# Optimization experiments

Hardware: AMD Instinct MI355X
Metric: run time of the kernel (lower is better)

## Reference

```python
import jax, jax.numpy as jnp
import numpy as np

B, T, D, UNITS = 32, 2048, 1024, 1024


def setup_inputs() -> dict:
    key = jax.random.key(0)
    ks = jax.random.split(key, 9)
    values = jax.random.normal(ks[0], (B, T, D), dtype=jnp.float32)
    query = jax.random.normal(ks[1], (B, D), dtype=jnp.float32)
    # mask: 1.0 where position is masked out, 0.0 otherwise
    mask = jax.random.randint(ks[2], (B, T), 0, 2).astype(jnp.float32)
    # Dense params (keras Dense: y = x @ W + b)
    W1 = jax.random.normal(ks[3], (D, UNITS), dtype=jnp.float32) / np.sqrt(D)
    b1 = jnp.zeros((UNITS,), dtype=jnp.float32)
    W2 = jax.random.normal(ks[4], (D, UNITS), dtype=jnp.float32) / np.sqrt(D)
    b2 = jnp.zeros((UNITS,), dtype=jnp.float32)
    V = jax.random.normal(ks[5], (UNITS, 1), dtype=jnp.float32) / np.sqrt(UNITS)
    bV = jnp.zeros((1,), dtype=jnp.float32)
    return {"values": values, "query": query, "mask": mask,
            "W1": W1, "b1": b1, "W2": W2, "b2": b2, "V": V, "bV": bV}


def reference(values, query, mask, W1, b1, W2, b2, V, bV):
    # values: [B,T,D], query: [B,D], mask: [B,T] (1.0 = masked)
    proj_v = jnp.einsum('btd,du->btu', values, W1) + b1          # [B,T,U]
    proj_q = (query @ W2 + b2)[:, None, :]                        # [B,1,U]
    score = jnp.tanh(proj_v + proj_q) @ V + bV                    # [B,T,1]
    score = score + mask[:, :, None] * (-1e9)                     # mask out
    attention_weights = jax.nn.softmax(score, axis=1)             # [B,T,1]
    context_vector = jnp.sum(attention_weights * values, axis=1)  # [B,D]
    return (context_vector, attention_weights)
```

## Files before the change

kernel.cpp:

```cpp
#include <hip/hip_runtime.h>
#include <hip/hip_bf16.h>


typedef __bf16 bf16x8 __attribute__((ext_vector_type(8)));
typedef __bf16 bf16x4 __attribute__((ext_vector_type(4)));
typedef short  s16x8  __attribute__((ext_vector_type(8)));
typedef float  f32x4  __attribute__((ext_vector_type(4)));

#define B_  32
#define T_  2048
#define D_  1024
#define U_  1024
#define BT_ (B_*T_)

#define WS_W1T    ((size_t)0)
#define WS_PROJQ  ((size_t)(2u*1024*1024))
#define WS_SCORE  ((size_t)(2u*1024*1024 + 128u*1024))
#define WS_VALB   ((size_t)(4u*1024*1024))
#define WS_NEEDED (WS_VALB + (size_t)BT_ * D_ * 2)

__device__ __forceinline__ float tanh_fast(float x) {
    const float e = __expf(2.0f * x);
    return 1.0f - __fdividef(2.0f, e + 1.0f);
}

__device__ __forceinline__ void glls16(const void* g, void* l) {
    __builtin_amdgcn_global_load_lds(
        (const __attribute__((address_space(1))) void*)g,
        (__attribute__((address_space(3))) void*)l, 16, 0, 0);
}

__global__ void init_kernel(const float* __restrict__ b1, const float* __restrict__ b2,
                            float* __restrict__ projq, float* __restrict__ score) {
    int i = blockIdx.x * 256 + threadIdx.x;
    if (i < B_ * U_) {
        projq[i] = b1[i & (U_ - 1)] + b2[i & (U_ - 1)];
    } else {
        score[i - B_ * U_] = 0.0f;
    }
}

__global__ void convert_kernel(const float* __restrict__ v, __bf16* __restrict__ o) {
    const size_t i = ((size_t)blockIdx.x * 256 + threadIdx.x) * 8;
    const float4 a = *(const float4*)(v + i);
    const float4 b = *(const float4*)(v + i + 4);
    bf16x8 h;
    h[0] = (__bf16)a.x; h[1] = (__bf16)a.y; h[2] = (__bf16)a.z; h[3] = (__bf16)a.w;
    h[4] = (__bf16)b.x; h[5] = (__bf16)b.y; h[6] = (__bf16)b.z; h[7] = (__bf16)b.w;
    *(bf16x8*)(o + i) = h;
}

__global__ void w1_transpose_kernel(const float* __restrict__ W1, __bf16* __restrict__ W1T) {
    __shared__ float tile[64][65];
    const int bx = blockIdx.x & 15;
    const int by = blockIdx.x >> 4;
    const int tid = threadIdx.x;
    const int j  = tid & 63;
    const int i0 = tid >> 6;
#pragma unroll
    for (int p = 0; p < 16; ++p) {
        const int i = i0 + p * 4;
        tile[i][j] = W1[(size_t)(by * 64 + i) * U_ + bx * 64 + j];
    }
    __syncthreads();
#pragma unroll
    for (int p = 0; p < 16; ++p) {
        const int i = i0 + p * 4;
        W1T[(size_t)(bx * 64 + i) * D_ + by * 64 + j] = (__bf16)tile[j][i];
    }
}

__global__ void projq_kernel(const float* __restrict__ query, const float* __restrict__ W2,
                             float* __restrict__ projq) {
    __shared__ float q[128];
    const int b  = blockIdx.x >> 3;
    const int dc = blockIdx.x & 7;
    const int tid = threadIdx.x;
    if (tid < 128) q[tid] = query[(size_t)b * D_ + dc * 128 + tid];
    __syncthreads();
    const int u0 = tid * 4;
    float a0 = 0.f, a1 = 0.f, a2 = 0.f, a3 = 0.f;
    for (int d = 0; d < 128; ++d) {
        const float4 w = *(const float4*)(W2 + (size_t)(dc * 128 + d) * U_ + u0);
        const float qd = q[d];
        a0 = fmaf(qd, w.x, a0); a1 = fmaf(qd, w.y, a1);
        a2 = fmaf(qd, w.z, a2); a3 = fmaf(qd, w.w, a3);
    }
    float* p = projq + (size_t)b * U_ + u0;
    atomicAdd(p + 0, a0); atomicAdd(p + 1, a1);
    atomicAdd(p + 2, a2); atomicAdd(p + 3, a3);
}


#define SC_LDSB 32768

__global__ __launch_bounds__(512, 2)
void score_kernel_8ph(const __bf16* __restrict__ valb, const __bf16* __restrict__ W1T,
                      const float* __restrict__ projq, const float* __restrict__ V,
                      float* __restrict__ score) {
    __shared__ __attribute__((aligned(16))) __bf16 lds[2 * SC_LDSB];

    const int tid  = threadIdx.x;
    const int bid  = blockIdx.x;
    const int xcd  = bid & 7;
    const int sl   = bid >> 3;
    const int mblk = xcd * 32 + (sl >> 2);
    const int nblk = sl & 3;

    const int wv   = tid >> 6;
    const int lane = tid & 63;
    const int wm   = wv >> 2;
    const int wn   = wv & 3;
    const int l15  = lane & 15, quad = lane >> 4;
    const int e    = l15 & 7;
    const int sl0  = ((quad)     ^ e) * 8;
    const int sl1  = ((quad + 4) ^ e) * 8;
    const int offA0 = wm * 8192 + l15 * 64 + sl0;
    const int offA1 = wm * 8192 + l15 * 64 + sl1;
    const int offB0 = 16384 + (wn >> 1) * 8192 + ((wn & 1) * 64 + l15) * 64 + sl0;
    const int offB1 = 16384 + (wn >> 1) * 8192 + ((wn & 1) * 64 + l15) * 64 + sl1;

    const int srow = lane >> 3;
    const int scol = ((lane & 7) ^ srow) * 8;
    const __bf16* aS = valb + ((size_t)mblk * 256 + wv * 8 + srow) * D_ + scol;
    const __bf16* bS = W1T  + ((size_t)nblk * 256 + wv * 8 + srow) * D_ + scol;
    __bf16* aD = lds + wv * 512;
    __bf16* bD = lds + 16384 + wv * 512;

#define DSR(dst, off) do { s16x8 _t;                                            \
    asm volatile("ds_read_b128 %0, %1" : "=v"(_t)                              \
        : "v"((const __attribute__((address_space(3))) __bf16*)(lds + (off)))); \
    (dst) = __builtin_bit_cast(bf16x8, _t); } while (0)

#define STA(CB, H, KT) do {                                                     \
    glls16(aS + (size_t)((H)*128     ) * D_ + (KT)*64, aD + (CB) + (H)*8192);        \
    glls16(aS + (size_t)((H)*128 + 64) * D_ + (KT)*64, aD + (CB) + (H)*8192 + 4096); \
    } while (0)
#define STB(CB, H, KT) do {                                                     \
    glls16(bS + (size_t)((H)*128     ) * D_ + (KT)*64, bD + (CB) + (H)*8192);        \
    glls16(bS + (size_t)((H)*128 + 64) * D_ + (KT)*64, bD + (CB) + (H)*8192 + 4096); \
    } while (0)

#define PH_SYNC do { __builtin_amdgcn_s_barrier();                              \
    asm volatile("s_waitcnt lgkmcnt(0)" ::: "memory");                          \
    __builtin_amdgcn_sched_barrier(0);                                          \
    __builtin_amdgcn_s_setprio(1); } while (0)
#define PH_END do { __builtin_amdgcn_s_setprio(0);                              \
    __builtin_amdgcn_s_barrier(); } while (0)

#define MQ(ML, NL) do {                                                         \
    _Pragma("unroll") for (int mi = 0; mi < 4; ++mi)                            \
    _Pragma("unroll") for (int ni = 0; ni < 2; ++ni) {                          \
        acc[(ML)+mi][(NL)+ni] = __builtin_amdgcn_mfma_f32_16x16x32_bf16(        \
            afr[mi][0], bfr[(NL)+ni][0], acc[(ML)+mi][(NL)+ni], 0, 0, 0);       \
        acc[(ML)+mi][(NL)+ni] = __builtin_amdgcn_mfma_f32_16x16x32_bf16(        \
            afr[mi][1], bfr[(NL)+ni][1], acc[(ML)+mi][(NL)+ni], 0, 0, 0);       \
    } } while (0)

#define TILE(KT, CB, DOA, DOB, VM) do {                                         \
                                 \
    _Pragma("unroll") for (int m = 0; m < 4; ++m) {                             \
        DSR(afr[m][0], (CB) + offA0 + m*1024);                                  \
        DSR(afr[m][1], (CB) + offA1 + m*1024); }                                \
    _Pragma("unroll") for (int n = 0; n < 2; ++n) {                             \
        DSR(bfr[n][0], (CB) + offB0 + n*1024);                                  \
        DSR(bfr[n][1], (CB) + offB1 + n*1024); }                                \
    if (DOA) STA((CB) ^ SC_LDSB, 0, (KT)+1);                                    \
    PH_SYNC; MQ(0, 0); PH_END;                                                  \
                                          \
    _Pragma("unroll") for (int n = 0; n < 2; ++n) {                             \
        DSR(bfr[2+n][0], (CB) + offB0 + (2+n)*1024);                            \
        DSR(bfr[2+n][1], (CB) + offB1 + (2+n)*1024); }                          \
    if (DOA) STA((CB) ^ SC_LDSB, 1, (KT)+1);                                    \
    PH_SYNC; MQ(0, 2); PH_END;                                                  \
                                          \
    _Pragma("unroll") for (int m = 0; m < 4; ++m) {                             \
        DSR(afr[m][0], (CB) + offA0 + (4+m)*1024);                              \
        DSR(afr[m][1], (CB) + offA1 + (4+m)*1024); }                            \
    if (DOB) STB((CB), 0, (KT)+2);                                              \
    PH_SYNC; MQ(4, 0); PH_END;                                                  \
             \
    if (DOB) STB((CB), 1, (KT)+2);                                              \
    __builtin_amdgcn_s_barrier();                                               \
    __builtin_amdgcn_sched_barrier(0);                                          \
    __builtin_amdgcn_s_setprio(1);                                              \
    MQ(4, 2);                                                                   \
    __builtin_amdgcn_s_setprio(0);                                              \
    if ((VM) == 4)      asm volatile("s_waitcnt vmcnt(4)" ::: "memory");        \
    else if ((VM) == 0) asm volatile("s_waitcnt vmcnt(0)" ::: "memory");        \
    __builtin_amdgcn_s_barrier();                                               \
} while (0)

    bf16x8 afr[4][2];
    bf16x8 bfr[4][2];
    f32x4  acc[8][4];
#pragma unroll
    for (int i = 0; i < 8; ++i)
#pragma unroll
        for (int j = 0; j < 4; ++j) { f32x4 z = {0.f, 0.f, 0.f, 0.f}; acc[i][j] = z; }

    STA(0, 0, 0); STA(0, 1, 0); STB(0, 0, 0); STB(0, 1, 0);
    STB(SC_LDSB, 0, 1); STB(SC_LDSB, 1, 1);
    asm volatile("s_waitcnt vmcnt(4)" ::: "memory");
    __builtin_amdgcn_s_barrier();

#pragma unroll 1
    for (int tt = 0; tt < 14; tt += 2) {
        TILE(tt,     0,       1, 1, 4);
        TILE(tt + 1, SC_LDSB, 1, 1, 4);
    }
    TILE(14, 0,       1, 0, 0);
    TILE(15, SC_LDSB, 0, 0, -1);

    const int bq = mblk >> 3;
    const float* pq = projq + (size_t)bq * U_ + nblk * 256 + wn * 64;
    const float* Vp = V + nblk * 256 + wn * 64;
    float pqu[4], vu[4];
#pragma unroll
    for (int nt = 0; nt < 4; ++nt) { pqu[nt] = pq[nt * 16 + l15]; vu[nt] = Vp[nt * 16 + l15]; }
    const size_t rowbase = (size_t)mblk * 256 + (size_t)wm * 128;
#pragma unroll
    for (int mt = 0; mt < 8; ++mt) {
        float s0 = 0.f, s1 = 0.f, s2 = 0.f, s3 = 0.f;
#pragma unroll
        for (int nt = 0; nt < 4; ++nt) {
            s0 += tanh_fast(acc[mt][nt][0] + pqu[nt]) * vu[nt];
            s1 += tanh_fast(acc[mt][nt][1] + pqu[nt]) * vu[nt];
            s2 += tanh_fast(acc[mt][nt][2] + pqu[nt]) * vu[nt];
            s3 += tanh_fast(acc[mt][nt][3] + pqu[nt]) * vu[nt];
        }
        float s[4] = {s0, s1, s2, s3};
#pragma unroll
        for (int r = 0; r < 4; ++r) {
            float v = s[r];
            v += __shfl_xor(v, 1);
            v += __shfl_xor(v, 2);
            v += __shfl_xor(v, 4);
            v += __shfl_xor(v, 8);
            if (l15 == 0)
                atomicAdd(&score[rowbase + mt * 16 + quad * 4 + r], v);
        }
    }
#undef DSR
#undef STA
#undef STB
#undef PH_SYNC
#undef PH_END
#undef MQ
#undef TILE
}

__global__ __launch_bounds__(512, 2)
void score_kernel_f32(const float* __restrict__ values, const __bf16* __restrict__ W1T,
                      const float* __restrict__ projq, const float* __restrict__ V,
                      float* __restrict__ score) {
    __shared__ __attribute__((aligned(16))) __bf16 Al[64][40];
    __shared__ __attribute__((aligned(16))) __bf16 Bl[512][40];
    const int tid    = threadIdx.x;
    const int rowblk = blockIdx.x >> 1;
    const int nhalf  = blockIdx.x & 1;
    const int wave = tid >> 6, lane = tid & 63;
    const int quad = lane >> 4, l15 = lane & 15;
    const float*  Abase = values + (size_t)rowblk * 64 * D_;
    const __bf16* Bbase = W1T + (size_t)nhalf * 512 * D_;
    const int ar = tid >> 3, ac = (tid & 7) * 4;
    const int br = tid >> 2, bc = (tid & 3) * 8;
    f32x4 acc[4][4];
#pragma unroll
    for (int i = 0; i < 4; ++i)
#pragma unroll
        for (int j = 0; j < 4; ++j) { f32x4 z = {0.f,0.f,0.f,0.f}; acc[i][j] = z; }
    for (int kk = 0; kk < D_; kk += 32) {
        {
            const float4 v = *(const float4*)(Abase + (size_t)ar * D_ + kk + ac);
            bf16x4 h;
            h[0] = (__bf16)v.x; h[1] = (__bf16)v.y; h[2] = (__bf16)v.z; h[3] = (__bf16)v.w;
            *(bf16x4*)(&Al[ar][ac]) = h;
        }
#pragma unroll
        for (int p = 0; p < 4; ++p) {
            const int rr = p * 128 + br;
            const bf16x8 w = *(const bf16x8*)(Bbase + (size_t)rr * D_ + kk + bc);
            *(bf16x8*)(&Bl[rr][bc]) = w;
        }
        __syncthreads();
        bf16x8 af[4];
#pragma unroll
        for (int mt = 0; mt < 4; ++mt)
            af[mt] = *(const bf16x8*)(&Al[mt * 16 + l15][quad * 8]);
#pragma unroll
        for (int nt = 0; nt < 4; ++nt) {
            const bf16x8 bfr = *(const bf16x8*)(&Bl[wave * 64 + nt * 16 + l15][quad * 8]);
#pragma unroll
            for (int mt = 0; mt < 4; ++mt)
                acc[mt][nt] = __builtin_amdgcn_mfma_f32_16x16x32_bf16(af[mt], bfr, acc[mt][nt], 0, 0, 0);
        }
        __syncthreads();
    }
    const int b = rowblk >> 5;
    const size_t rowbase = (size_t)rowblk * 64;
    const float* pq = projq + (size_t)b * U_;
    const int ub = nhalf * 512 + wave * 64;
#pragma unroll
    for (int mt = 0; mt < 4; ++mt) {
        float s0 = 0.f, s1 = 0.f, s2 = 0.f, s3 = 0.f;
#pragma unroll
        for (int nt = 0; nt < 4; ++nt) {
            const int u = ub + nt * 16 + l15;
            const float pqu = pq[u];
            const float vu  = V[u];
            s0 += tanh_fast(acc[mt][nt][0] + pqu) * vu;
            s1 += tanh_fast(acc[mt][nt][1] + pqu) * vu;
            s2 += tanh_fast(acc[mt][nt][2] + pqu) * vu;
            s3 += tanh_fast(acc[mt][nt][3] + pqu) * vu;
        }
        float s[4] = {s0, s1, s2, s3};
#pragma unroll
        for (int r = 0; r < 4; ++r) {
            float v = s[r];
            v += __shfl_xor(v, 1);
            v += __shfl_xor(v, 2);
            v += __shfl_xor(v, 4);
            v += __shfl_xor(v, 8);
            if (l15 == 0)
                atomicAdd(&score[rowbase + mt * 16 + quad * 4 + r], v);
        }
    }
}

__global__ void softmax_kernel(const float* __restrict__ score, const float* __restrict__ mask,
                               const float* __restrict__ bV, float* __restrict__ out) {
    const int b = blockIdx.x;
    const int tid = threadIdx.x;
    const float bv = bV[0];
    float s[8];
    float lmax = -3.0e38f;
#pragma unroll
    for (int i = 0; i < 8; ++i) {
        const int t = tid + i * 256;
        const float v = score[(size_t)b * T_ + t] + bv + mask[(size_t)b * T_ + t] * (-1.0e9f);
        s[i] = v;
        lmax = fmaxf(lmax, v);
    }
#pragma unroll
    for (int m = 1; m < 64; m <<= 1) lmax = fmaxf(lmax, __shfl_xor(lmax, m));
    __shared__ float redm[4], reds[4];
    if ((tid & 63) == 0) redm[tid >> 6] = lmax;
    __syncthreads();
    const float M = fmaxf(fmaxf(redm[0], redm[1]), fmaxf(redm[2], redm[3]));
    float lsum = 0.f;
#pragma unroll
    for (int i = 0; i < 8; ++i) { s[i] = __expf(s[i] - M); lsum += s[i]; }
#pragma unroll
    for (int m = 1; m < 64; m <<= 1) lsum += __shfl_xor(lsum, m);
    if ((tid & 63) == 0) reds[tid >> 6] = lsum;
    __syncthreads();
    const float inv = 1.0f / (reds[0] + reds[1] + reds[2] + reds[3]);
#pragma unroll
    for (int i = 0; i < 8; ++i)
        out[(size_t)B_ * D_ + (size_t)b * T_ + tid + i * 256] = s[i] * inv;
}

__global__ void context_kernel(const float* __restrict__ values, const float* __restrict__ attn,
                               float* __restrict__ out) {
    const int b  = blockIdx.x >> 4;
    const int dc = blockIdx.x & 15;
    const int tid = threadIdx.x;
    __shared__ float a[T_];
#pragma unroll
    for (int i = 0; i < 8; ++i) a[tid + i * 256] = attn[(size_t)b * T_ + tid + i * 256];
    __syncthreads();
    const int dl = (tid & 15) * 4;
    const int tg = tid >> 4;
    const float* vb = values + (size_t)b * T_ * D_ + dc * 64 + dl;
    f32x4 acc = {0.f, 0.f, 0.f, 0.f};
#pragma unroll 4
    for (int t = tg; t < T_; t += 16) {
        const float4 v = *(const float4*)(vb + (size_t)t * D_);
        const float w = a[t];
        acc[0] = fmaf(w, v.x, acc[0]);
        acc[1] = fmaf(w, v.y, acc[1]);
        acc[2] = fmaf(w, v.z, acc[2]);
        acc[3] = fmaf(w, v.w, acc[3]);
    }
    __shared__ __attribute__((aligned(16))) float red[16][64];
    *(f32x4*)(&red[tg][dl]) = acc;
    __syncthreads();
    if (tid < 64) {
        float s = 0.f;
#pragma unroll
        for (int g = 0; g < 16; ++g) s += red[g][tid];
        out[(size_t)b * D_ + dc * 64 + tid] = s;
    }
}

extern "C" void kernel_launch(void* const* d_in, const int* in_sizes, int n_in,
                              void* d_out, int out_size, void* d_ws, size_t ws_size,
                              hipStream_t stream) {
    const float* values = (const float*)d_in[0];
    const float* query  = (const float*)d_in[1];
    const float* mask   = (const float*)d_in[2];
    const float* W1     = (const float*)d_in[3];
    const float* b1     = (const float*)d_in[4];
    const float* W2     = (const float*)d_in[5];
    const float* b2     = (const float*)d_in[6];
    const float* V      = (const float*)d_in[7];
    const float* bV     = (const float*)d_in[8];
    float* out = (float*)d_out;

    char* ws = (char*)d_ws;
    __bf16* W1T   = (__bf16*)(ws + WS_W1T);
    float*  projq = (float*)(ws + WS_PROJQ);
    float*  score = (float*)(ws + WS_SCORE);
    __bf16* valb  = (__bf16*)(ws + WS_VALB);

    init_kernel<<<dim3(384), dim3(256), 0, stream>>>(b1, b2, projq, score);
    w1_transpose_kernel<<<dim3(256), dim3(256), 0, stream>>>(W1, W1T);
    projq_kernel<<<dim3(256), dim3(256), 0, stream>>>(query, W2, projq);
    if (ws_size >= WS_NEEDED) {
        convert_kernel<<<dim3(32768), dim3(256), 0, stream>>>(values, valb);
        score_kernel_8ph<<<dim3(1024), dim3(512), 0, stream>>>(valb, W1T, projq, V, score);
    } else {
        score_kernel_f32<<<dim3(2048), dim3(512), 0, stream>>>(values, W1T, projq, V, score);
    }
    softmax_kernel<<<dim3(32), dim3(256), 0, stream>>>(score, mask, bV, out);
    context_kernel<<<dim3(512), dim3(256), 0, stream>>>(values, out + B_ * D_, out);
}
```

Before: 615.4 us.

## Register-double-buffer score GEMM fragments and read bf16 values in context kernel

The score GEMM main loop is restructured so A fragments alternate between two register sets (afA/afB). The next tile's first fragments are prefetched from LDS before the current tile finishes, and the per-phase double barriers are replaced with finer lgkmcnt waits. This aims to hide LDS read latency behind MFMA work and cut barrier stalls, at the cost of more VGPR pressure at two waves per SIMD. Separately, the context reduction now reads the bf16 copy of values, halving its bytes read but accumulating from rounded inputs.

Result: slower. 849.5 us (+38.0%).

```diff
diff --git a/kernel.cpp b/kernel.cpp
--- a/kernel.cpp
+++ b/kernel.cpp
@@ -95,9 +95,9 @@
 #define SC_LDSB 32768
 
 __global__ __launch_bounds__(512, 2)
-void score_kernel_8ph(const __bf16* __restrict__ valb, const __bf16* __restrict__ W1T,
-                      const float* __restrict__ projq, const float* __restrict__ V,
-                      float* __restrict__ score) {
+void score_kernel_ra(const __bf16* __restrict__ valb, const __bf16* __restrict__ W1T,
+                     const float* __restrict__ projq, const float* __restrict__ V,
+                     float* __restrict__ score) {
     __shared__ __attribute__((aligned(16))) __bf16 lds[2 * SC_LDSB];
 
     const int tid  = threadIdx.x;
@@ -141,57 +141,58 @@
     glls16(bS + (size_t)((H)*128 + 64) * D_ + (KT)*64, bD + (CB) + (H)*8192 + 4096); \
     } while (0)
 
-#define PH_SYNC do { __builtin_amdgcn_s_barrier();                              \
-    asm volatile("s_waitcnt lgkmcnt(0)" ::: "memory");                          \
-    __builtin_amdgcn_sched_barrier(0);                                          \
-    __builtin_amdgcn_s_setprio(1); } while (0)
-#define PH_END do { __builtin_amdgcn_s_setprio(0);                              \
-    __builtin_amdgcn_s_barrier(); } while (0)
-
-#define MQ(ML, NL) do {                                                         \
+#define MQG(AF, ML, NL) do {                                                    \
     _Pragma("unroll") for (int mi = 0; mi < 4; ++mi)                            \
     _Pragma("unroll") for (int ni = 0; ni < 2; ++ni) {                          \
         acc[(ML)+mi][(NL)+ni] = __builtin_amdgcn_mfma_f32_16x16x32_bf16(        \
-            afr[mi][0], bfr[(NL)+ni][0], acc[(ML)+mi][(NL)+ni], 0, 0, 0);       \
+            AF[mi][0], bfr[(NL)+ni][0], acc[(ML)+mi][(NL)+ni], 0, 0, 0);        \
         acc[(ML)+mi][(NL)+ni] = __builtin_amdgcn_mfma_f32_16x16x32_bf16(        \
-            afr[mi][1], bfr[(NL)+ni][1], acc[(ML)+mi][(NL)+ni], 0, 0, 0);       \
+            AF[mi][1], bfr[(NL)+ni][1], acc[(ML)+mi][(NL)+ni], 0, 0, 0);        \
     } } while (0)
 
-#define TILE(KT, CB, DOA, DOB, VM) do {                                         \
-                                 \
+#define TILE(KT, CB, DOA, DOB, VMS, DORD) do {                                  \
+                                                                       \
+    DSR(bfr[2][0], (CB) + offB0 + 2*1024);                                      \
+    DSR(bfr[2][1], (CB) + offB1 + 2*1024);                                      \
+    DSR(bfr[3][0], (CB) + offB0 + 3*1024);                                      \
+    DSR(bfr[3][1], (CB) + offB1 + 3*1024);                                      \
+    if (DOA) STA((CB) ^ SC_LDSB, 0, (KT) + 1);                                  \
+    asm volatile("s_waitcnt lgkmcnt(4)" ::: "memory");                          \
+    __builtin_amdgcn_sched_barrier(0);                                          \
+    __builtin_amdgcn_s_setprio(1); MQG(afA, 0, 0); __builtin_amdgcn_s_setprio(0);\
+                                                                       \
     _Pragma("unroll") for (int m = 0; m < 4; ++m) {                             \
-        DSR(afr[m][0], (CB) + offA0 + m*1024);                                  \
-        DSR(afr[m][1], (CB) + offA1 + m*1024); }                                \
-    _Pragma("unroll") for (int n = 0; n < 2; ++n) {                             \
-        DSR(bfr[n][0], (CB) + offB0 + n*1024);                                  \
-        DSR(bfr[n][1], (CB) + offB1 + n*1024); }                                \
-    if (DOA) STA((CB) ^ SC_LDSB, 0, (KT)+1);                                    \
-    PH_SYNC; MQ(0, 0); PH_END;                                                  \
-                                          \
-    _Pragma("unroll") for (int n = 0; n < 2; ++n) {                             \
-        DSR(bfr[2+n][0], (CB) + offB0 + (2+n)*1024);                            \
-        DSR(bfr[2+n][1], (CB) + offB1 + (2+n)*1024); }                          \
-    if (DOA) STA((CB) ^ SC_LDSB, 1, (KT)+1);                                    \
-    PH_SYNC; MQ(0, 2); PH_END;                                                  \
-                                          \
-    _Pragma("unroll") for (int m = 0; m < 4; ++m) {                             \
-        DSR(afr[m][0], (CB) + offA0 + (4+m)*1024);                              \
-        DSR(afr[m][1], (CB) + offA1 + (4+m)*1024); }                            \
-    if (DOB) STB((CB), 0, (KT)+2);                                              \
-    PH_SYNC; MQ(4, 0); PH_END;                                                  \
-             \
-    if (DOB) STB((CB), 1, (KT)+2);                                              \
+        DSR(afB[m][0], (CB) + offA0 + (4 + m) * 1024);                          \
+        DSR(afB[m][1], (CB) + offA1 + (4 + m) * 1024); }                        \
+    if (DOA) STA((CB) ^ SC_LDSB, 1, (KT) + 1);                                  \
+    asm volatile("s_waitcnt lgkmcnt(8)" ::: "memory");                          \
+    __builtin_amdgcn_sched_barrier(0);                                          \
+    __builtin_amdgcn_s_setprio(1); MQG(afA, 0, 2); __builtin_amdgcn_s_setprio(0);\
     __builtin_amdgcn_s_barrier();                                               \
+                                                                       \
+    if (DOB) STB((CB), 0, (KT) + 2);                                            \
+    asm volatile("s_waitcnt lgkmcnt(0)" ::: "memory");                          \
     __builtin_amdgcn_sched_barrier(0);                                          \
-    __builtin_amdgcn_s_setprio(1);                                              \
-    MQ(4, 2);                                                                   \
-    __builtin_amdgcn_s_setprio(0);                                              \
-    if ((VM) == 4)      asm volatile("s_waitcnt vmcnt(4)" ::: "memory");        \
-    else if ((VM) == 0) asm volatile("s_waitcnt vmcnt(0)" ::: "memory");        \
+    __builtin_amdgcn_s_setprio(1); MQG(afB, 4, 0); __builtin_amdgcn_s_setprio(0);\
+    asm volatile("s_waitcnt vmcnt(" VMS ")" ::: "memory");                      \
     __builtin_amdgcn_s_barrier();                                               \
+                                                                       \
+    if (DORD) {                                                                 \
+        _Pragma("unroll") for (int m = 0; m < 4; ++m) {                         \
+            DSR(afA[m][0], ((CB) ^ SC_LDSB) + offA0 + m * 1024);                \
+            DSR(afA[m][1], ((CB) ^ SC_LDSB) + offA1 + m * 1024); }              \
+        DSR(bfr[0][0], ((CB) ^ SC_LDSB) + offB0);                               \
+        DSR(bfr[0][1], ((CB) ^ SC_LDSB) + offB1);                               \
+        DSR(bfr[1][0], ((CB) ^ SC_LDSB) + offB0 + 1024);                        \
+        DSR(bfr[1][1], ((CB) ^ SC_LDSB) + offB1 + 1024);                        \
+    }                                                                           \
+    if (DOB) STB((CB), 1, (KT) + 2);                                            \
+    __builtin_amdgcn_sched_barrier(0);                                          \
+    __builtin_amdgcn_s_setprio(1); MQG(afB, 4, 2); __builtin_amdgcn_s_setprio(0);\
 } while (0)
 
-    bf16x8 afr[4][2];
+    bf16x8 afA[4][2];
+    bf16x8 afB[4][2];
     bf16x8 bfr[4][2];
     f32x4  acc[8][4];
 #pragma unroll
@@ -203,14 +204,21 @@
     STB(SC_LDSB, 0, 1); STB(SC_LDSB, 1, 1);
     asm volatile("s_waitcnt vmcnt(4)" ::: "memory");
     __builtin_amdgcn_s_barrier();
+#pragma unroll
+    for (int m = 0; m < 4; ++m) {
+        DSR(afA[m][0], offA0 + m * 1024);
+        DSR(afA[m][1], offA1 + m * 1024);
+    }
+    DSR(bfr[0][0], offB0);        DSR(bfr[0][1], offB1);
+    DSR(bfr[1][0], offB0 + 1024); DSR(bfr[1][1], offB1 + 1024);
 
 #pragma unroll 1
     for (int tt = 0; tt < 14; tt += 2) {
-        TILE(tt,     0,       1, 1, 4);
-        TILE(tt + 1, SC_LDSB, 1, 1, 4);
-    }
-    TILE(14, 0,       1, 0, 0);
-    TILE(15, SC_LDSB, 0, 0, -1);
+        TILE(tt,     0,       1, 1, "2", 1);
+        TILE(tt + 1, SC_LDSB, 1, 1, "2", 1);
+    }
+    TILE(14, 0,       1, 0, "0", 1);
+    TILE(15, SC_LDSB, 0, 0, "0", 0);
 
     const int bq = mblk >> 3;
     const float* pq = projq + (size_t)bq * U_ + nblk * 256 + wn * 64;
@@ -244,9 +252,7 @@
 #undef DSR
 #undef STA
 #undef STB
-#undef PH_SYNC
-#undef PH_END
-#undef MQ
+#undef MQG
 #undef TILE
 }
 
@@ -361,6 +367,40 @@
         out[(size_t)B_ * D_ + (size_t)b * T_ + tid + i * 256] = s[i] * inv;
 }
 
+__global__ void context_kernel_bf16(const __bf16* __restrict__ valb, const float* __restrict__ attn,
+                                    float* __restrict__ out) {
+    const int b  = blockIdx.x >> 4;
+    const int dc = blockIdx.x & 15;
+    const int tid = threadIdx.x;
+    __shared__ float a[T_];
+#pragma unroll
+    for (int i = 0; i < 8; ++i) a[tid + i * 256] = attn[(size_t)b * T_ + tid + i * 256];
+    __syncthreads();
+    const int dl = (tid & 7) * 8;
+    const int tg = tid >> 3;
+    const __bf16* vb = valb + (size_t)b * T_ * D_ + dc * 64 + dl;
+    float acc[8];
+#pragma unroll
+    for (int j = 0; j < 8; ++j) acc[j] = 0.f;
+#pragma unroll 4
+    for (int t = tg; t < T_; t += 32) {
+        const bf16x8 v = *(const bf16x8*)(vb + (size_t)t * D_);
+        const float w = a[t];
+#pragma unroll
+        for (int j = 0; j < 8; ++j) acc[j] = fmaf(w, (float)v[j], acc[j]);
+    }
+    __shared__ __attribute__((aligned(16))) float red[32][65];
+#pragma unroll
+    for (int j = 0; j < 8; ++j) red[tg][dl + j] = acc[j];
+    __syncthreads();
+    if (tid < 64) {
+        float s = 0.f;
+#pragma unroll
+        for (int g = 0; g < 32; ++g) s += red[g][tid];
+        out[(size_t)b * D_ + dc * 64 + tid] = s;
+    }
+}
+
 __global__ void context_kernel(const float* __restrict__ values, const float* __restrict__ attn,
                                float* __restrict__ out) {
     const int b  = blockIdx.x >> 4;
@@ -419,10 +459,12 @@
     projq_kernel<<<dim3(256), dim3(256), 0, stream>>>(query, W2, projq);
     if (ws_size >= WS_NEEDED) {
         convert_kernel<<<dim3(32768), dim3(256), 0, stream>>>(values, valb);
-        score_kernel_8ph<<<dim3(1024), dim3(512), 0, stream>>>(valb, W1T, projq, V, score);
+        score_kernel_ra<<<dim3(1024), dim3(512), 0, stream>>>(valb, W1T, projq, V, score);
+        softmax_kernel<<<dim3(32), dim3(256), 0, stream>>>(score, mask, bV, out);
+        context_kernel_bf16<<<dim3(512), dim3(256), 0, stream>>>(valb, out + B_ * D_, out);
     } else {
         score_kernel_f32<<<dim3(2048), dim3(512), 0, stream>>>(values, W1T, projq, V, score);
-    }
-    softmax_kernel<<<dim3(32), dim3(256), 0, stream>>>(score, mask, bV, out);
-    context_kernel<<<dim3(512), dim3(256), 0, stream>>>(values, out + B_ * D_, out);
-}
+        softmax_kernel<<<dim3(32), dim3(256), 0, stream>>>(score, mask, bV, out);
+        context_kernel<<<dim3(512), dim3(256), 0, stream>>>(values, out + B_ * D_, out);
+    }
+}
```
